# Optimization experiments

Measured on AMD Instinct MI355X. Metric: run time of the kernel, lower is better.

Reference implementation:

```python
import jax, jax.numpy as jnp
import numpy as np

N_PTS = 32768      # n_x == n_y (query points == source points)
K_NBR = 32         # neighbors per query point
N_EDGES = N_PTS * K_NBR
D_COORD = 3
C = 64             # f_y channels == MLP output channels
H = 256            # MLP hidden width


def setup_inputs() -> dict:
    key = jax.random.key(0)
    ks = jax.random.split(key, 12)
    y = jax.random.normal(ks[0], (N_PTS, D_COORD), dtype=jnp.float32)
    x = jax.random.normal(ks[1], (N_PTS, D_COORD), dtype=jnp.float32)
    f_y = jax.random.normal(ks[2], (N_PTS, C), dtype=jnp.float32)
    neighbors_index = jax.random.randint(ks[3], (N_EDGES,), 0, N_PTS, dtype=jnp.int64)
    neighbors_row_splits = (jnp.arange(N_PTS + 1, dtype=jnp.int64) * K_NBR)
    weights = jax.random.uniform(ks[4], (N_EDGES,), dtype=jnp.float32)
    # LinearChannelMLP params: layers [6, 256, 256, 64], gelu between layers
    def dense(k, fan_in, fan_out):
        w = jax.random.normal(k, (fan_in, fan_out), dtype=jnp.float32) / np.sqrt(fan_in)
        return w
    W0 = dense(ks[5], 2 * D_COORD, H)
    b0 = jnp.zeros((H,), dtype=jnp.float32)
    W1 = dense(ks[6], H, H)
    b1 = jnp.zeros((H,), dtype=jnp.float32)
    W2 = dense(ks[7], H, C)
    b2 = jnp.zeros((C,), dtype=jnp.float32)
    return {"y": y, "x": x, "f_y": f_y,
            "neighbors_index": neighbors_index,
            "neighbors_row_splits": neighbors_row_splits,
            "weights": weights,
            "W0": W0, "b0": b0, "W1": W1, "b1": b1, "W2": W2, "b2": b2}


def reference(y, x, f_y, neighbors_index, neighbors_row_splits, weights,
              W0, b0, W1, b1, W2, b2):
    n_x = neighbors_row_splits.shape[0] - 1
    n_edges = neighbors_index.shape[0]
    # CSR row id for each edge (equivalent to repeat(arange(n_x), num_reps))
    seg = jnp.searchsorted(neighbors_row_splits, jnp.arange(n_edges), side='right') - 1
    rep_features = y[neighbors_index]            # [E, 3] gathered source coords
    self_features = x[seg]                       # [E, 3] repeated query coords
    agg = jnp.concatenate([rep_features, self_features], axis=-1)  # [E, 6]
    # channel MLP (gelu between layers, none after last)
    h = jax.nn.gelu(agg @ W0 + b0)
    h = jax.nn.gelu(h @ W1 + b1)
    rep = h @ W2 + b2                            # [E, C] kernel values
    # transform_type='linear': kernel * f_y(neighbor)
    rep = rep * f_y[neighbors_index]
    # quadrature weights (forces sum reduction, as in source)
    rep = rep * weights[:, None]
    out = jax.ops.segment_sum(rep, seg, num_segments=n_x)  # segment-CSR sum
    return out
```

## Files before the change

### kernel.cpp

```cpp
#include <hip/hip_runtime.h>
#include <hip/hip_bf16.h>
#include <stdint.h>

#define NPTS 32768
#define KNBR 32
#define NEDGES (NPTS * KNBR)
#define TM 64
#define AGG_STRIDE 40
#define H_STRIDE 264

typedef __attribute__((ext_vector_type(8))) short short8;
typedef __attribute__((ext_vector_type(4))) float f32x4;
typedef __attribute__((ext_vector_type(4))) unsigned int u32x4;
typedef __attribute__((ext_vector_type(2))) unsigned int u32x2;

__device__ __forceinline__ unsigned short f2bf(float f) {
    unsigned int u = __float_as_uint(f);
    unsigned int r = (u + 0x7FFFu + ((u >> 16) & 1u)) >> 16;
    return (unsigned short)r;
}

__device__ __forceinline__ unsigned int cvt_pk_bf16(float lo, float hi) {
    unsigned int r;
    asm("v_cvt_pk_bf16_f32 %0, %1, %2" : "=v"(r) : "v"(lo), "v"(hi));
    return r;
}

__device__ __forceinline__ float gelu_tanh(float x) {
    float x2 = x * x;
    float u = fmaf(-0.102942496f, x2, -2.30220824f);
    float e = __builtin_amdgcn_exp2f(x * u);
    return x * __builtin_amdgcn_rcpf(1.0f + e);
}

__global__ void pack_w(const float* __restrict__ W0, const float* __restrict__ W1,
                       const float* __restrict__ W2, unsigned short* __restrict__ wp) {
    int tid = blockIdx.x * blockDim.x + threadIdx.x;
    if (tid >= 176 * 64) return;
    int fid = tid >> 6, l = tid & 63, ln = l & 15, lg = l >> 4;
    unsigned short v[8];
    if (fid < 16) {
        int nt = fid, k0 = lg * 8;
        #pragma unroll
        for (int j = 0; j < 8; ++j) {
            int k = k0 + j;
            v[j] = f2bf(k < 6 ? W0[k * 256 + nt * 16 + ln] : 0.0f);
        }
    } else if (fid < 144) {
        int g = fid - 16;
        int wn = g >> 6, rem = g & 63, s = rem >> 3, n = rem & 7;
        int col = (wn * 8 + n) * 16 + ln;
        int k0 = s * 32 + lg * 8;
        #pragma unroll
        for (int j = 0; j < 8; ++j) v[j] = f2bf(W1[(k0 + j) * 256 + col]);
    } else {
        int g = fid - 144;
        int c = g >> 3, s = g & 7;
        int col = c * 16 + ln;
        int k0 = s * 32 + lg * 8;
        #pragma unroll
        for (int j = 0; j < 8; ++j) v[j] = f2bf(W2[(k0 + j) * 64 + col]);
    }
    unsigned short* o = &wp[tid * 8];
    #pragma unroll
    for (int j = 0; j < 8; ++j) o[j] = v[j];
}

__global__ __launch_bounds__(256, 3)
void gno_fused(const float* __restrict__ y, const float* __restrict__ x,
               const float* __restrict__ f_y, const int* __restrict__ nbr,
               const float* __restrict__ wts,
               const float* __restrict__ b0, const float* __restrict__ b1,
               const float* __restrict__ b2,
               const unsigned short* __restrict__ wp,
               float* __restrict__ out) {
    __shared__ __align__(16) unsigned short agg_lds[TM * AGG_STRIDE];
    __shared__ __align__(16) unsigned short h_lds[TM * H_STRIDE];

    const int b = blockIdx.x;
    const int tid = threadIdx.x;
    const int l = tid & 63;
    const int w = tid >> 6;
    const int wm = w & 1;
    const int wn = w >> 1;
    const int lg = l >> 4;
    const int ln = l & 15;
    const int ebase = b * TM;

    const char* wpb = (const char*)wp;
    const char* pW0 = wpb + wn * 8192 + l * 16;
    const char* pW1 = wpb + 16384 + wn * 65536 + l * 16;
    const char* pW2 = wpb + 147456 + wn * 16384 + l * 16;
    const char* aggb = (const char*)agg_lds + (wm * 32 + ln) * (AGG_STRIDE * 2) + lg * 16;
    char* hwb = (char*)h_lds + (wm * 32 + ln) * (H_STRIDE * 2) + wn * 256 + lg * 8;
    const char* hrb = (const char*)h_lds + (wm * 32 + ln) * (H_STRIDE * 2) + lg * 16;

    if (tid < TM) {
        int e = ebase + tid;
        int j = nbr[e];
        int i = e >> 5;
        const float* yr = &y[j * 3];
        const float* xr = &x[i * 3];
        u32x4 q0;
        q0.x = cvt_pk_bf16(yr[0], yr[1]);
        q0.y = cvt_pk_bf16(yr[2], xr[0]);
        q0.z = cvt_pk_bf16(xr[1], xr[2]);
        q0.w = 0u;
        u32x4 z = {0u, 0u, 0u, 0u};
        unsigned short* row = &agg_lds[tid * AGG_STRIDE];
        *(u32x4*)(row +  0) = q0;
        *(u32x4*)(row +  8) = z;
        *(u32x4*)(row + 16) = z;
        *(u32x4*)(row + 24) = z;
    }
    __syncthreads();

    {
        short8 ag[2];
        #pragma unroll
        for (int m = 0; m < 2; ++m)
            ag[m] = *(const short8*)(aggb + m * 1280);
        #pragma unroll
        for (int n = 0; n < 8; ++n) {
            short8 aw = *(const short8*)(pW0 + n * 1024);
            f32x4 b0f = *(const f32x4*)&b0[(8 * wn + n) * 16 + lg * 4];
            #pragma unroll
            for (int m = 0; m < 2; ++m) {
                f32x4 c = __builtin_amdgcn_mfma_f32_16x16x32_bf16(aw, ag[m], b0f, 0, 0, 0);
                u32x2 pv;
                pv.x = cvt_pk_bf16(gelu_tanh(c[0]), gelu_tanh(c[1]));
                pv.y = cvt_pk_bf16(gelu_tanh(c[2]), gelu_tanh(c[3]));
                *(u32x2*)(hwb + m * 8448 + n * 32) = pv;
            }
        }
    }
    __syncthreads();

    f32x4 acc[2][8];
    #pragma unroll
    for (int n = 0; n < 8; ++n) {
        f32x4 b1f = *(const f32x4*)&b1[(8 * wn + n) * 16 + lg * 4];
        acc[0][n] = b1f;
        acc[1][n] = b1f;
    }
    #pragma unroll
    for (int s = 0; s < 8; ++s) {
        short8 hb[2];
        #pragma unroll
        for (int m = 0; m < 2; ++m)
            hb[m] = *(const short8*)(hrb + m * 8448 + s * 64);
        #pragma unroll
        for (int n = 0; n < 8; ++n) {
            short8 aw = *(const short8*)(pW1 + (s * 8 + n) * 1024);
            #pragma unroll
            for (int m = 0; m < 2; ++m)
                acc[m][n] = __builtin_amdgcn_mfma_f32_16x16x32_bf16(aw, hb[m], acc[m][n], 0, 0, 0);
        }
    }
    __syncthreads();

    #pragma unroll
    for (int n = 0; n < 8; ++n) {
        #pragma unroll
        for (int m = 0; m < 2; ++m) {
            u32x2 pv;
            pv.x = cvt_pk_bf16(gelu_tanh(acc[m][n][0]), gelu_tanh(acc[m][n][1]));
            pv.y = cvt_pk_bf16(gelu_tanh(acc[m][n][2]), gelu_tanh(acc[m][n][3]));
            *(u32x2*)(hwb + m * 8448 + n * 32) = pv;
        }
    }
    __syncthreads();

    f32x4 acc3[2][2];
    #pragma unroll
    for (int jj = 0; jj < 2; ++jj) {
        f32x4 b2f = *(const f32x4*)&b2[(2 * wn + jj) * 16 + lg * 4];
        acc3[0][jj] = b2f;
        acc3[1][jj] = b2f;
    }
    #pragma unroll
    for (int s = 0; s < 8; ++s) {
        short8 hb[2];
        #pragma unroll
        for (int m = 0; m < 2; ++m)
            hb[m] = *(const short8*)(hrb + m * 8448 + s * 64);
        #pragma unroll
        for (int jj = 0; jj < 2; ++jj) {
            short8 aw = *(const short8*)(pW2 + (jj * 8 + s) * 1024);
            #pragma unroll
            for (int m = 0; m < 2; ++m)
                acc3[m][jj] = __builtin_amdgcn_mfma_f32_16x16x32_bf16(aw, hb[m], acc3[m][jj], 0, 0, 0);
        }
    }

    {
        f32x4 seg[2];
        seg[0] = (f32x4){0.f, 0.f, 0.f, 0.f};
        seg[1] = (f32x4){0.f, 0.f, 0.f, 0.f};
        #pragma unroll
        for (int m = 0; m < 2; ++m) {
            int e = ebase + (2 * wm + m) * 16 + ln;
            int j = nbr[e];
            float wt = wts[e];
            #pragma unroll
            for (int jj = 0; jj < 2; ++jj) {
                int ch = (2 * wn + jj) * 16 + lg * 4;
                f32x4 fy = *(const f32x4*)&f_y[j * 64 + ch];
                f32x4 v;
                #pragma unroll
                for (int i = 0; i < 4; ++i)
                    v[i] = acc3[m][jj][i] * fy[i] * wt;
                seg[jj] += v;
            }
        }
        #pragma unroll
        for (int jj = 0; jj < 2; ++jj) {
            f32x4 v = seg[jj];
            #pragma unroll
            for (int d = 1; d <= 8; d <<= 1) {
                #pragma unroll
                for (int i = 0; i < 4; ++i)
                    v[i] += __shfl_xor(v[i], d, 64);
            }
            if (ln == 0)
                *(f32x4*)&out[(2 * b + wm) * 64 + (2 * wn + jj) * 16 + lg * 4] = v;
        }
    }
}

extern "C" void kernel_launch(void* const* d_in, const int* in_sizes, int n_in,
                              void* d_out, int out_size, void* d_ws, size_t ws_size,
                              hipStream_t stream) {
    const float* y   = (const float*)d_in[0];
    const float* x   = (const float*)d_in[1];
    const float* f_y = (const float*)d_in[2];
    const int*   nbr = (const int*)d_in[3];
    const float* wts = (const float*)d_in[5];
    const float* W0  = (const float*)d_in[6];
    const float* b0  = (const float*)d_in[7];
    const float* W1  = (const float*)d_in[8];
    const float* b1  = (const float*)d_in[9];
    const float* W2  = (const float*)d_in[10];
    const float* b2  = (const float*)d_in[11];
    unsigned short* wp = (unsigned short*)d_ws;
    float* out = (float*)d_out;

    pack_w<<<dim3(44), dim3(256), 0, stream>>>(W0, W1, W2, wp);
    gno_fused<<<dim3(NEDGES / TM), dim3(256), 0, stream>>>(
        y, x, f_y, nbr, wts, b0, b1, b2, wp, out);
}
```

Measured before the change: 290.3 us.

## Double edge tile to 128 with 8 waves, each wave owning all rows and 32 cols

```diff
diff --git a/kernel.cpp b/kernel.cpp
--- a/kernel.cpp
+++ b/kernel.cpp
@@ -5,7 +5,7 @@
 #define NPTS 32768
 #define KNBR 32
 #define NEDGES (NPTS * KNBR)
-#define TM 64
+#define TM 128
 #define AGG_STRIDE 40
 #define H_STRIDE 264
 
@@ -48,8 +48,8 @@
         }
     } else if (fid < 144) {
         int g = fid - 16;
-        int wn = g >> 6, rem = g & 63, s = rem >> 3, n = rem & 7;
-        int col = (wn * 8 + n) * 16 + ln;
+        int nt = g >> 3, s = g & 7;
+        int col = nt * 16 + ln;
         int k0 = s * 32 + lg * 8;
         #pragma unroll
         for (int j = 0; j < 8; ++j) v[j] = f2bf(W1[(k0 + j) * 256 + col]);
@@ -66,7 +66,7 @@
     for (int j = 0; j < 8; ++j) o[j] = v[j];
 }
 
-__global__ __launch_bounds__(256, 3)
+__global__ __launch_bounds__(512, 4)
 void gno_fused(const float* __restrict__ y, const float* __restrict__ x,
                const float* __restrict__ f_y, const int* __restrict__ nbr,
                const float* __restrict__ wts,
@@ -82,18 +82,18 @@
     const int l = tid & 63;
     const int w = tid >> 6;
     const int wm = w & 1;
-    const int wn = w >> 1;
+    const int wc = w >> 1;
     const int lg = l >> 4;
     const int ln = l & 15;
     const int ebase = b * TM;
 
     const char* wpb = (const char*)wp;
-    const char* pW0 = wpb + wn * 8192 + l * 16;
-    const char* pW1 = wpb + 16384 + wn * 65536 + l * 16;
-    const char* pW2 = wpb + 147456 + wn * 16384 + l * 16;
-    const char* aggb = (const char*)agg_lds + (wm * 32 + ln) * (AGG_STRIDE * 2) + lg * 16;
-    char* hwb = (char*)h_lds + (wm * 32 + ln) * (H_STRIDE * 2) + wn * 256 + lg * 8;
-    const char* hrb = (const char*)h_lds + (wm * 32 + ln) * (H_STRIDE * 2) + lg * 16;
+    const char* pW0 = wpb + w * 2048 + l * 16;
+    const char* pW1 = wpb + 16384 + w * 16384 + l * 16;
+    const char* pW2 = wpb + 147456 + wc * 8192 + l * 16;
+    const char* aggb = (const char*)agg_lds + ln * 80 + lg * 16;
+    char* hwb = (char*)h_lds + ln * 528 + w * 64 + lg * 8;
+    const char* hrb = (const char*)h_lds + ln * 528 + lg * 16;
 
     if (tid < TM) {
         int e = ebase + tid;
@@ -116,80 +116,82 @@
     __syncthreads();
 
     {
-        short8 ag[2];
-        #pragma unroll
-        for (int m = 0; m < 2; ++m)
-            ag[m] = *(const short8*)(aggb + m * 1280);
-        #pragma unroll
-        for (int n = 0; n < 8; ++n) {
-            short8 aw = *(const short8*)(pW0 + n * 1024);
-            f32x4 b0f = *(const f32x4*)&b0[(8 * wn + n) * 16 + lg * 4];
-            #pragma unroll
-            for (int m = 0; m < 2; ++m) {
-                f32x4 c = __builtin_amdgcn_mfma_f32_16x16x32_bf16(aw, ag[m], b0f, 0, 0, 0);
-                u32x2 pv;
-                pv.x = cvt_pk_bf16(gelu_tanh(c[0]), gelu_tanh(c[1]));
-                pv.y = cvt_pk_bf16(gelu_tanh(c[2]), gelu_tanh(c[3]));
-                *(u32x2*)(hwb + m * 8448 + n * 32) = pv;
-            }
-        }
-    }
-    __syncthreads();
-
-    f32x4 acc[2][8];
-    #pragma unroll
-    for (int n = 0; n < 8; ++n) {
-        f32x4 b1f = *(const f32x4*)&b1[(8 * wn + n) * 16 + lg * 4];
-        acc[0][n] = b1f;
-        acc[1][n] = b1f;
+        short8 aw0 = *(const short8*)(pW0);
+        short8 aw1 = *(const short8*)(pW0 + 1024);
+        f32x4 b0f0 = *(const f32x4*)&b0[(2 * w) * 16 + lg * 4];
+        f32x4 b0f1 = *(const f32x4*)&b0[(2 * w + 1) * 16 + lg * 4];
+        #pragma unroll
+        for (int mt = 0; mt < 8; ++mt) {
+            short8 ag = *(const short8*)(aggb + mt * 1280);
+            f32x4 c0 = __builtin_amdgcn_mfma_f32_16x16x32_bf16(aw0, ag, b0f0, 0, 0, 0);
+            f32x4 c1 = __builtin_amdgcn_mfma_f32_16x16x32_bf16(aw1, ag, b0f1, 0, 0, 0);
+            u32x2 p0, p1;
+            p0.x = cvt_pk_bf16(gelu_tanh(c0[0]), gelu_tanh(c0[1]));
+            p0.y = cvt_pk_bf16(gelu_tanh(c0[2]), gelu_tanh(c0[3]));
+            p1.x = cvt_pk_bf16(gelu_tanh(c1[0]), gelu_tanh(c1[1]));
+            p1.y = cvt_pk_bf16(gelu_tanh(c1[2]), gelu_tanh(c1[3]));
+            *(u32x2*)(hwb + mt * 8448)      = p0;
+            *(u32x2*)(hwb + mt * 8448 + 32) = p1;
+        }
+    }
+    __syncthreads();
+
+    f32x4 acc[8][2];
+    {
+        f32x4 b1f0 = *(const f32x4*)&b1[(2 * w) * 16 + lg * 4];
+        f32x4 b1f1 = *(const f32x4*)&b1[(2 * w + 1) * 16 + lg * 4];
+        #pragma unroll
+        for (int mt = 0; mt < 8; ++mt) { acc[mt][0] = b1f0; acc[mt][1] = b1f1; }
     }
     #pragma unroll
     for (int s = 0; s < 8; ++s) {
-        short8 hb[2];
-        #pragma unroll
-        for (int m = 0; m < 2; ++m)
-            hb[m] = *(const short8*)(hrb + m * 8448 + s * 64);
-        #pragma unroll
-        for (int n = 0; n < 8; ++n) {
-            short8 aw = *(const short8*)(pW1 + (s * 8 + n) * 1024);
-            #pragma unroll
-            for (int m = 0; m < 2; ++m)
-                acc[m][n] = __builtin_amdgcn_mfma_f32_16x16x32_bf16(aw, hb[m], acc[m][n], 0, 0, 0);
-        }
-    }
-    __syncthreads();
-
-    #pragma unroll
-    for (int n = 0; n < 8; ++n) {
-        #pragma unroll
-        for (int m = 0; m < 2; ++m) {
+        short8 aw0 = *(const short8*)(pW1 + s * 1024);
+        short8 aw1 = *(const short8*)(pW1 + 8192 + s * 1024);
+        #pragma unroll
+        for (int mt = 0; mt < 8; ++mt) {
+            short8 hb = *(const short8*)(hrb + mt * 8448 + s * 64);
+            acc[mt][0] = __builtin_amdgcn_mfma_f32_16x16x32_bf16(aw0, hb, acc[mt][0], 0, 0, 0);
+            acc[mt][1] = __builtin_amdgcn_mfma_f32_16x16x32_bf16(aw1, hb, acc[mt][1], 0, 0, 0);
+        }
+    }
+    __syncthreads();
+
+    #pragma unroll
+    for (int mt = 0; mt < 8; ++mt) {
+        #pragma unroll
+        for (int n = 0; n < 2; ++n) {
             u32x2 pv;
-            pv.x = cvt_pk_bf16(gelu_tanh(acc[m][n][0]), gelu_tanh(acc[m][n][1]));
-            pv.y = cvt_pk_bf16(gelu_tanh(acc[m][n][2]), gelu_tanh(acc[m][n][3]));
-            *(u32x2*)(hwb + m * 8448 + n * 32) = pv;
-        }
-    }
-    __syncthreads();
-
-    f32x4 acc3[2][2];
-    #pragma unroll
-    for (int jj = 0; jj < 2; ++jj) {
-        f32x4 b2f = *(const f32x4*)&b2[(2 * wn + jj) * 16 + lg * 4];
-        acc3[0][jj] = b2f;
-        acc3[1][jj] = b2f;
-    }
+            pv.x = cvt_pk_bf16(gelu_tanh(acc[mt][n][0]), gelu_tanh(acc[mt][n][1]));
+            pv.y = cvt_pk_bf16(gelu_tanh(acc[mt][n][2]), gelu_tanh(acc[mt][n][3]));
+            *(u32x2*)(hwb + mt * 8448 + n * 32) = pv;
+        }
+    }
+    __syncthreads();
+
+    f32x4 fy[4];
+    float wv[4];
+    #pragma unroll
+    for (int m = 0; m < 4; ++m) {
+        int e = ebase + (wm * 4 + m) * 16 + ln;
+        int j = nbr[e];
+        fy[m] = *(const f32x4*)&f_y[j * 64 + wc * 16 + lg * 4];
+        wv[m] = wts[e];
+    }
+
+    f32x4 acc3[4];
+    {
+        f32x4 b2f = *(const f32x4*)&b2[wc * 16 + lg * 4];
+        #pragma unroll
+        for (int m = 0; m < 4; ++m) acc3[m] = b2f;
+    }
+    const char* hrb3 = hrb + wm * 33792;
     #pragma unroll
     for (int s = 0; s < 8; ++s) {
-        short8 hb[2];
-        #pragma unroll
-        for (int m = 0; m < 2; ++m)
-            hb[m] = *(const short8*)(hrb + m * 8448 + s * 64);
-        #pragma unroll
-        for (int jj = 0; jj < 2; ++jj) {
-            short8 aw = *(const short8*)(pW2 + (jj * 8 + s) * 1024);
-            #pragma unroll
-            for (int m = 0; m < 2; ++m)
-                acc3[m][jj] = __builtin_amdgcn_mfma_f32_16x16x32_bf16(aw, hb[m], acc3[m][jj], 0, 0, 0);
+        short8 aw = *(const short8*)(pW2 + s * 1024);
+        #pragma unroll
+        for (int m = 0; m < 4; ++m) {
+            short8 hb = *(const short8*)(hrb3 + m * 8448 + s * 64);
+            acc3[m] = __builtin_amdgcn_mfma_f32_16x16x32_bf16(aw, hb, acc3[m], 0, 0, 0);
         }
     }
 
@@ -198,24 +200,16 @@
         seg[0] = (f32x4){0.f, 0.f, 0.f, 0.f};
         seg[1] = (f32x4){0.f, 0.f, 0.f, 0.f};
         #pragma unroll
-        for (int m = 0; m < 2; ++m) {
-            int e = ebase + (2 * wm + m) * 16 + ln;
-            int j = nbr[e];
-            float wt = wts[e];
+        for (int m = 0; m < 4; ++m) {
+            f32x4 v;
             #pragma unroll
-            for (int jj = 0; jj < 2; ++jj) {
-                int ch = (2 * wn + jj) * 16 + lg * 4;
-                f32x4 fy = *(const f32x4*)&f_y[j * 64 + ch];
-                f32x4 v;
-                #pragma unroll
-                for (int i = 0; i < 4; ++i)
-                    v[i] = acc3[m][jj][i] * fy[i] * wt;
-                seg[jj] += v;
-            }
-        }
-        #pragma unroll
-        for (int jj = 0; jj < 2; ++jj) {
-            f32x4 v = seg[jj];
+            for (int i = 0; i < 4; ++i)
+                v[i] = acc3[m][i] * fy[m][i] * wv[m];
+            seg[m >> 1] += v;
+        }
+        #pragma unroll
+        for (int g = 0; g < 2; ++g) {
+            f32x4 v = seg[g];
             #pragma unroll
             for (int d = 1; d <= 8; d <<= 1) {
                 #pragma unroll
@@ -223,7 +217,7 @@
                     v[i] += __shfl_xor(v[i], d, 64);
             }
             if (ln == 0)
-                *(f32x4*)&out[(2 * b + wm) * 64 + (2 * wn + jj) * 16 + lg * 4] = v;
+                *(f32x4*)&out[(b * 4 + wm * 2 + g) * 64 + wc * 16 + lg * 4] = v;
         }
     }
 }
@@ -246,6 +240,6 @@
     float* out = (float*)d_out;
 
     pack_w<<<dim3(44), dim3(256), 0, stream>>>(W0, W1, W2, wp);
-    gno_fused<<<dim3(NEDGES / TM), dim3(256), 0, stream>>>(
+    gno_fused<<<dim3(NEDGES / TM), dim3(512), 0, stream>>>(
         y, x, f_y, nbr, wts, b0, b1, b2, wp, out);
 }
```

Result: faster. 257.4 us (-11.4%).
